# Optimization experiments

Hardware: AMD Instinct MI355X
Metric: run time of the kernel (lower is better)

Reference implementation:

```python
import jax, jax.numpy as jnp
import numpy as np

B, E, K, S, D, H, C = 8192, 8, 2, 32, 3072, 256, 100  # batch, experts, fix_points, img size, flat dim, hidden, classes


def setup_inputs() -> dict:
    key = jax.random.key(0)
    ks = jax.random.split(key, 6)
    return {
        "x": jax.random.normal(ks[0], (B, 3, S, S), jnp.float32),
        "coeffs_t": jax.random.uniform(ks[1], (K,), jnp.float32),
        "router_w": jax.random.normal(ks[2], (K, D, E), jnp.float32) * 0.02,
        "router_b": jnp.zeros((K, E), jnp.float32),
        "w1": jax.random.normal(ks[3], (E, K, D, H), jnp.float32) * 0.02,
        "b1": jnp.zeros((E, K, H), jnp.float32),
        "w2": jax.random.normal(ks[4], (E, K, H, C), jnp.float32) * 0.02,
        "b2": jnp.zeros((E, K, C), jnp.float32),
    }


def reference(x, coeffs_t, router_w, router_b, w1, b1, w2, b2):
    xf = x.reshape(x.shape[0], -1)  # [B, D]
    # Curve parameter blend: W = sum_k coeffs_t[k] * W_k (CurveParameter semantics)
    Wr = jnp.einsum('k,kde->de', coeffs_t, router_w)
    br = jnp.einsum('k,ke->e', coeffs_t, router_b)
    # Router: top-1 expert index per sample
    idx = jnp.argmax(xf @ Wr + br, axis=-1)  # [B] int
    # Blended expert weights
    W1 = jnp.einsum('k,ekdh->edh', coeffs_t, w1)
    B1 = jnp.einsum('k,ekh->eh', coeffs_t, b1)
    W2 = jnp.einsum('k,ekhc->ehc', coeffs_t, w2)
    B2 = jnp.einsum('k,ekc->ec', coeffs_t, b2)
    # Expert MLP (computed for all experts with static shapes, then top-1 gather;
    # identical math to torch's boolean-mask dispatch/scatter)
    h = jax.nn.gelu(jnp.einsum('bd,edh->beh', xf, W1) + B1, approximate=False)  # [B,E,H]
    o = jnp.einsum('beh,ehc->bec', h, W2) + B2  # [B,E,C]
    return jnp.take_along_axis(o, idx[:, None, None], axis=1)[:, 0, :]  # [B,C]
```

## Files before the change

kernel.cpp:

```cpp
#include <hip/hip_runtime.h>
#include <math.h>

#define B_  8192
#define E_  8
#define D_  3072
#define H_  256
#define C_  100
#define DH_ (D_*H_)
#define HC_ (H_*C_)
#define KS_ 8
#define KSEG_ (D_/KS_)
#define NTMAX_ 136

typedef __attribute__((ext_vector_type(4))) float  f32x4;
typedef __attribute__((ext_vector_type(8))) __bf16 bf16x8;
typedef __attribute__((ext_vector_type(8))) unsigned short ush8;
typedef __attribute__((ext_vector_type(4))) unsigned short ush4;

__device__ inline unsigned short bf16_rne(float f) {
    unsigned u = __builtin_bit_cast(unsigned, f);
    unsigned r = (u + 0x7FFFu + ((u >> 16) & 1u)) >> 16;
    return (unsigned short)r;
}
__device__ inline float bf16_f(unsigned short h) {
    unsigned u = ((unsigned)h) << 16;
    return __builtin_bit_cast(float, u);
}

#define MISC_B1_ (E_*H_/4)
#define MISC_B2_ (E_*C_/4)
#define MISC_TOT_ (MISC_B1_ + MISC_B2_ + D_)
__global__ __launch_bounds__(256) void blend_misc_k(
        const float* __restrict__ b1, const float* __restrict__ b2,
        const float* __restrict__ rw, float* __restrict__ B1b,
        float* __restrict__ B2b, double* __restrict__ wsd,
        const float* __restrict__ coeffs) {
    int gid = blockIdx.x * 256 + threadIdx.x;
    float c0 = coeffs[0], c1 = coeffs[1];
    if (gid < MISC_B1_) {
        const float4* p = (const float4*)b1;
        int e = gid / (H_ / 4), r = gid - e * (H_ / 4);
        float4 a = p[(e * 2 + 0) * (H_ / 4) + r];
        float4 bq = p[(e * 2 + 1) * (H_ / 4) + r];
        float4 o;
        o.x = c0 * a.x + c1 * bq.x;
        o.y = c0 * a.y + c1 * bq.y;
        o.z = c0 * a.z + c1 * bq.z;
        o.w = c0 * a.w + c1 * bq.w;
        ((float4*)B1b)[gid] = o;
    } else if (gid < MISC_B1_ + MISC_B2_) {
        int g2 = gid - MISC_B1_;
        const float4* p = (const float4*)b2;
        int e = g2 / (C_ / 4), r = g2 - e * (C_ / 4);
        float4 a = p[(e * 2 + 0) * (C_ / 4) + r];
        float4 bq = p[(e * 2 + 1) * (C_ / 4) + r];
        float4 o;
        o.x = c0 * a.x + c1 * bq.x;
        o.y = c0 * a.y + c1 * bq.y;
        o.z = c0 * a.z + c1 * bq.z;
        o.w = c0 * a.w + c1 * bq.w;
        ((float4*)B2b)[g2] = o;
    } else {
        int d = gid - (MISC_B1_ + MISC_B2_);
        if (d < D_) {
            double c0d = (double)c0, c1d = (double)c1;
            #pragma unroll
            for (int ee = 0; ee < 8; ee++)
                wsd[(size_t)d * 8 + ee] = c0d * (double)rw[(size_t)d * 8 + ee]
                                        + c1d * (double)rw[(size_t)(D_ + d) * 8 + ee];
        }
    }
}

#define TP_ 136
__global__ __launch_bounds__(256) void blendw1t_k(
        const float* __restrict__ w1, unsigned short* __restrict__ Whi,
        unsigned short* __restrict__ Wlo, const float* __restrict__ coeffs) {
    __shared__ unsigned short thi[64 * TP_];
    __shared__ unsigned short tlo[64 * TP_];
    float c0 = coeffs[0], c1 = coeffs[1];
    int t = threadIdx.x;
    int e = blockIdx.z, h0 = blockIdx.y * 64, d0 = blockIdx.x * 128;
    int h = t & 63, dl = t >> 6;
    const float* pa = w1 + ((size_t)(e * 2 + 0) * D_ + d0) * H_ + h0 + h;
    const float* pb = w1 + ((size_t)(e * 2 + 1) * D_ + d0) * H_ + h0 + h;
    for (int it = 0; it < 32; it++) {
        int d = it * 4 + dl;
        float v = c0 * pa[(size_t)d * H_] + c1 * pb[(size_t)d * H_];
        unsigned short hi = bf16_rne(v);
        thi[h * TP_ + d] = hi;
        tlo[h * TP_ + d] = bf16_rne(v - bf16_f(hi));
    }
    __syncthreads();
    #pragma unroll
    for (int it = 0; it < 4; it++) {
        int i = t + it * 256;
        int hh = i >> 4, d8 = (i & 15) * 8;
        size_t g = (size_t)(e * H_ + h0 + hh) * D_ + d0 + d8;
        *(ush8*)(Whi + g) = *(const ush8*)&thi[hh * TP_ + d8];
        *(ush8*)(Wlo + g) = *(const ush8*)&tlo[hh * TP_ + d8];
    }
}

__global__ __launch_bounds__(256) void blendw2t_k(
        const float* __restrict__ w2, unsigned short* __restrict__ W2thi,
        unsigned short* __restrict__ W2tlo, const float* __restrict__ coeffs) {
    float c0 = coeffs[0], c1 = coeffs[1];
    int c = blockIdx.x, e = blockIdx.y, k = threadIdx.x;
    float v = c0 * w2[((size_t)(e * 2 + 0) * H_ + k) * C_ + c]
            + c1 * w2[((size_t)(e * 2 + 1) * H_ + k) * C_ + c];
    unsigned short hi = bf16_rne(v);
    W2thi[(size_t)(e * C_ + c) * H_ + k] = hi;
    W2tlo[(size_t)(e * C_ + c) * H_ + k] = bf16_rne(v - bf16_f(hi));
}

template<int RKS>
__global__ __launch_bounds__(64) void router_v2_t(
        const float* __restrict__ x, const double* __restrict__ wsd,
        double* __restrict__ lpart) {
    const int RSEG = D_ / RKS;
    __shared__ float  xs[64][33];
    __shared__ double wls[32][8];
    int lane = threadIdx.x;
    int row0 = blockIdx.x * 64;
    int kbase = blockIdx.y * RSEG;

    double acc[8] = {0, 0, 0, 0, 0, 0, 0, 0};

    for (int kb = 0; kb < RSEG; kb += 32) {
        #pragma unroll
        for (int it = 0; it < 8; it++) {
            int i = lane + it * 64;
            int r = i >> 3, c4 = i & 7;
            *(float4*)&xs[r][c4 * 4] =
                *(const float4*)(x + (size_t)(row0 + r) * D_ + kbase + kb + c4 * 4);
        }
        #pragma unroll
        for (int it = 0; it < 4; it++) {
            int i = lane + it * 64;
            int k = i >> 3, ee = i & 7;
            wls[k][ee] = wsd[(size_t)(kbase + kb + k) * 8 + ee];
        }
        __syncthreads();
        #pragma unroll
        for (int kk = 0; kk < 32; kk++) {
            double xv = (double)xs[lane][kk];
            double2 w01 = *(const double2*)&wls[kk][0];
            double2 w23 = *(const double2*)&wls[kk][2];
            double2 w45 = *(const double2*)&wls[kk][4];
            double2 w67 = *(const double2*)&wls[kk][6];
            acc[0] = fma(xv, w01.x, acc[0]);
            acc[1] = fma(xv, w01.y, acc[1]);
            acc[2] = fma(xv, w23.x, acc[2]);
            acc[3] = fma(xv, w23.y, acc[3]);
            acc[4] = fma(xv, w45.x, acc[4]);
            acc[5] = fma(xv, w45.y, acc[5]);
            acc[6] = fma(xv, w67.x, acc[6]);
            acc[7] = fma(xv, w67.y, acc[7]);
        }
        __syncthreads();
    }
    size_t base = ((size_t)blockIdx.y * B_ + row0 + lane) * 8;
    #pragma unroll
    for (int ee = 0; ee < 8; ee++) lpart[base + ee] = acc[ee];
}

template<int RKS>
__global__ __launch_bounds__(256) void argmax_t(
        const double* __restrict__ lpart, const float* __restrict__ rb,
        const float* __restrict__ coeffs, int* __restrict__ idx,
        int* __restrict__ cnt) {
    __shared__ int scnt[8];
    int t = threadIdx.x;
    if (t < 8) scnt[t] = 0;
    __syncthreads();
    int b = blockIdx.x * 256 + t;
    double c0 = (double)coeffs[0], c1 = (double)coeffs[1];
    double best = -1e300;
    int bi = 0;
    #pragma unroll
    for (int e = 0; e < 8; e++) {
        double l = c0 * (double)rb[e] + c1 * (double)rb[8 + e];
        #pragma unroll
        for (int s2 = 0; s2 < RKS; s2++)
            l += lpart[((size_t)s2 * B_ + b) * 8 + e];
        if (l > best) { best = l; bi = e; }
    }
    idx[b] = bi;
    atomicAdd(&scnt[bi], 1);
    __syncthreads();
    if (t < 8 && scnt[t] > 0) atomicAdd(&cnt[t], scnt[t]);
}

__global__ void offsets_k(const int* __restrict__ cnt, int* __restrict__ off,
                          int* __restrict__ cursor, int* __restrict__ tmap,
                          int* __restrict__ ntl) {
    if (threadIdx.x == 0) {
        int s = 0;
        for (int e = 0; e < E_; e++) { off[e] = s; cursor[e] = s; s += cnt[e]; }
        int nt = 0;
        for (int e = 0; e < E_; e++)
            for (int t0 = 0; t0 < cnt[e]; t0 += 64)
                tmap[nt++] = (e << 16) | t0;
        ntl[0] = nt;
    }
}

__global__ void scatter_k(const int* __restrict__ idx, int* __restrict__ cursor,
                          int* __restrict__ order) {
    int b = blockIdx.x * blockDim.x + threadIdx.x;
    if (b < B_) {
        int e = idx[b];
        int pos = atomicAdd(&cursor[e], 1);
        order[pos] = (e << 16) | b;
    }
}

template<int MODE>
__global__ __launch_bounds__(256, 3) void gemm1_t(
        const float* __restrict__ x, const unsigned short* __restrict__ Whi,
        const unsigned short* __restrict__ Wlo, const int* __restrict__ order,
        const int* __restrict__ cnt, const int* __restrict__ off,
        const int* __restrict__ tmap, const int* __restrict__ ntl,
        float* __restrict__ dst) {
    int tid = blockIdx.y;
    if (tid >= ntl[0]) return;
    int tm = tmap[tid];
    int e = tm >> 16, tile0 = tm & 0xFFFF;
    int ce = cnt[e];
    int s = blockIdx.x;

    __shared__ int rows[64];
    __shared__ unsigned short xs_hi[64 * 40];
    __shared__ unsigned short xs_lo[64 * 40];
    __shared__ unsigned short ws_hi[256 * 40];
    __shared__ unsigned short ws_lo[256 * 40];

    int t = threadIdx.x;
    if (t < 64) {
        int i = tile0 + t;
        rows[t] = (i < ce) ? (order[off[e] + i] & 0xFFFF) : -1;
    }
    __syncthreads();
    int xrow0 = rows[0];

    int lane = t & 63, w = t >> 6;
    int lr = lane & 15, quad = lane >> 4;
    int kbase = s * KSEG_;

    f32x4 acc[4][4];
    #pragma unroll
    for (int mt = 0; mt < 4; mt++)
        #pragma unroll
        for (int nt = 0; nt < 4; nt++)
            acc[mt][nt] = (f32x4){0.f, 0.f, 0.f, 0.f};

    for (int kb = 0; kb < KSEG_; kb += 32) {
        #pragma unroll
        for (int it = 0; it < 2; it++) {
            int i = t + it * 256;
            int rr = i >> 3, sg = i & 7;
            int row = rows[rr];
            if (row < 0) row = xrow0;
            float4 v = *(const float4*)(x + (size_t)row * D_ + kbase + kb + sg * 4);
            unsigned short h4[4], l4[4];
            float vv[4] = {v.x, v.y, v.z, v.w};
            #pragma unroll
            for (int j = 0; j < 4; j++) {
                unsigned short hi = bf16_rne(vv[j]);
                h4[j] = hi;
                l4[j] = bf16_rne(vv[j] - bf16_f(hi));
            }
            *(ush4*)&xs_hi[rr * 40 + sg * 4] = *(const ush4*)h4;
            *(ush4*)&xs_lo[rr * 40 + sg * 4] = *(const ush4*)l4;
        }
        #pragma unroll
        for (int it = 0; it < 4; it++) {
            int i = t + it * 256;
            int col = i >> 2, ch = i & 3;
            size_t g = (size_t)(e * H_ + col) * D_ + kbase + kb + ch * 8;
            *(ush8*)&ws_hi[col * 40 + ch * 8] = *(const ush8*)(Whi + g);
            *(ush8*)&ws_lo[col * 40 + ch * 8] = *(const ush8*)(Wlo + g);
        }
        __syncthreads();

        bf16x8 ah[4], al[4], bh[4], bl[4];
        #pragma unroll
        for (int mt = 0; mt < 4; mt++) {
            ah[mt] = __builtin_bit_cast(bf16x8, *(const ush8*)&xs_hi[(mt * 16 + lr) * 40 + quad * 8]);
            al[mt] = __builtin_bit_cast(bf16x8, *(const ush8*)&xs_lo[(mt * 16 + lr) * 40 + quad * 8]);
        }
        #pragma unroll
        for (int nt = 0; nt < 4; nt++) {
            int col = w * 64 + nt * 16 + lr;
            bh[nt] = __builtin_bit_cast(bf16x8, *(const ush8*)&ws_hi[col * 40 + quad * 8]);
            bl[nt] = __builtin_bit_cast(bf16x8, *(const ush8*)&ws_lo[col * 40 + quad * 8]);
        }
        #pragma unroll
        for (int mt = 0; mt < 4; mt++)
            #pragma unroll
            for (int nt = 0; nt < 4; nt++) {
                acc[mt][nt] = __builtin_amdgcn_mfma_f32_16x16x32_bf16(ah[mt], bh[nt], acc[mt][nt], 0, 0, 0);
                acc[mt][nt] = __builtin_amdgcn_mfma_f32_16x16x32_bf16(al[mt], bh[nt], acc[mt][nt], 0, 0, 0);
                acc[mt][nt] = __builtin_amdgcn_mfma_f32_16x16x32_bf16(ah[mt], bl[nt], acc[mt][nt], 0, 0, 0);
                acc[mt][nt] = __builtin_amdgcn_mfma_f32_16x16x32_bf16(al[mt], bl[nt], acc[mt][nt], 0, 0, 0);
            }
        __syncthreads();
    }

    size_t p0 = (size_t)off[e] + tile0;
    if (MODE == 1) {
        float* dp = dst + ((size_t)s * B_ + p0) * H_;
        #pragma unroll
        for (int mt = 0; mt < 4; mt++) {
            int rl = mt * 16 + quad * 4;
            #pragma unroll
            for (int nt = 0; nt < 4; nt++) {
                int col = w * 64 + nt * 16 + lr;
                #pragma unroll
                for (int rg = 0; rg < 4; rg++) {
                    if (tile0 + rl + rg < ce)
                        dp[(size_t)(rl + rg) * H_ + col] = acc[mt][nt][rg];
                }
            }
        }
    } else {
        #pragma unroll
        for (int mt = 0; mt < 4; mt++) {
            int rl = mt * 16 + quad * 4;
            #pragma unroll
            for (int nt = 0; nt < 4; nt++) {
                int col = w * 64 + nt * 16 + lr;
                #pragma unroll
                for (int rg = 0; rg < 4; rg++) {
                    if (tile0 + rl + rg < ce)
                        atomicAdd(&dst[(p0 + rl + rg) * H_ + col], acc[mt][nt][rg]);
                }
            }
        }
    }
}

__global__ __launch_bounds__(256) void reduce_gelu_k(
        float* __restrict__ hpart, const float* __restrict__ B1b,
        const int* __restrict__ order) {
    int gid = blockIdx.x * 256 + threadIdx.x;
    int p = gid >> 6, c4 = (gid & 63) * 4;
    int e = order[p] >> 16;
    size_t o = (size_t)p * H_ + c4;
    float4 a = *(const float4*)(hpart + o);
    #pragma unroll
    for (int s2 = 1; s2 < KS_; s2++) {
        float4 b = *(const float4*)(hpart + (size_t)s2 * B_ * H_ + o);
        a.x += b.x; a.y += b.y; a.z += b.z; a.w += b.w;
    }
    const float4 bb = *(const float4*)(B1b + e * H_ + c4);
    float pre[4] = {a.x + bb.x, a.y + bb.y, a.z + bb.z, a.w + bb.w};
    float4 og;
    og.x = 0.5f * pre[0] * (1.0f + erff(pre[0] * 0.70710678118654752440f));
    og.y = 0.5f * pre[1] * (1.0f + erff(pre[1] * 0.70710678118654752440f));
    og.z = 0.5f * pre[2] * (1.0f + erff(pre[2] * 0.70710678118654752440f));
    og.w = 0.5f * pre[3] * (1.0f + erff(pre[3] * 0.70710678118654752440f));
    *(float4*)(hpart + o) = og;
}

__global__ __launch_bounds__(256) void bias_gelu_k(
        float* __restrict__ hws, const float* __restrict__ B1b,
        const int* __restrict__ order) {
    int gid = blockIdx.x * 256 + threadIdx.x;
    int p = gid >> 6, c4 = (gid & 63) * 4;
    int e = order[p] >> 16;
    float4 v = *(const float4*)(hws + (size_t)p * H_ + c4);
    const float4 bb = *(const float4*)(B1b + e * H_ + c4);
    float pre[4] = {v.x + bb.x, v.y + bb.y, v.z + bb.z, v.w + bb.w};
    float4 o;
    o.x = 0.5f * pre[0] * (1.0f + erff(pre[0] * 0.70710678118654752440f));
    o.y = 0.5f * pre[1] * (1.0f + erff(pre[1] * 0.70710678118654752440f));
    o.z = 0.5f * pre[2] * (1.0f + erff(pre[2] * 0.70710678118654752440f));
    o.w = 0.5f * pre[3] * (1.0f + erff(pre[3] * 0.70710678118654752440f));
    *(float4*)(hws + (size_t)p * H_ + c4) = o;
}

__global__ __launch_bounds__(256) void gemm2_k(
        const float* __restrict__ hws,
        const unsigned short* __restrict__ W2thi, const unsigned short* __restrict__ W2tlo,
        const float* __restrict__ B2b, const int* __restrict__ order,
        const int* __restrict__ cnt, const int* __restrict__ off,
        const int* __restrict__ tmap, const int* __restrict__ ntl,
        float* __restrict__ out) {
    int tid = blockIdx.x;
    if (tid >= ntl[0]) return;
    int tm = tmap[tid];
    int e = tm >> 16, tile0 = tm & 0xFFFF;
    int ce = cnt[e];

    __shared__ int rows[64];
    int t = threadIdx.x;
    if (t < 64) {
        int i = tile0 + t;
        rows[t] = (i < ce) ? (order[off[e] + i] & 0xFFFF) : -1;
    }
    __syncthreads();

    int lane = t & 63, w = t >> 6;
    int m = lane & 15, q = lane >> 4;
    int lr = w * 16 + m;
    int p = off[e] + tile0 + ((tile0 + lr < ce) ? lr : 0);

    f32x4 acc[7];
    #pragma unroll
    for (int nt = 0; nt < 7; nt++) acc[nt] = (f32x4){0.f, 0.f, 0.f, 0.f};

    const unsigned short* w2h = W2thi + (size_t)e * C_ * H_;
    const unsigned short* w2l = W2tlo + (size_t)e * C_ * H_;

    #pragma unroll
    for (int s = 0; s < 8; s++) {
        float4 v0 = *(const float4*)(hws + (size_t)p * H_ + s * 32 + q * 8);
        float4 v1 = *(const float4*)(hws + (size_t)p * H_ + s * 32 + q * 8 + 4);
        float f[8] = {v0.x, v0.y, v0.z, v0.w, v1.x, v1.y, v1.z, v1.w};
        unsigned short hh[8], lo[8];
        #pragma unroll
        for (int j = 0; j < 8; j++) {
            unsigned short hi = bf16_rne(f[j]);
            hh[j] = hi;
            lo[j] = bf16_rne(f[j] - bf16_f(hi));
        }
        bf16x8 ah = __builtin_bit_cast(bf16x8, *(const ush8*)hh);
        bf16x8 al = __builtin_bit_cast(bf16x8, *(const ush8*)lo);
        #pragma unroll
        for (int nt = 0; nt < 7; nt++) {
            size_t bo = (size_t)(nt * 16 + m) * H_ + s * 32 + q * 8;
            bf16x8 bh = __builtin_bit_cast(bf16x8, *(const ush8*)(w2h + bo));
            bf16x8 bl = __builtin_bit_cast(bf16x8, *(const ush8*)(w2l + bo));
            acc[nt] = __builtin_amdgcn_mfma_f32_16x16x32_bf16(ah, bh, acc[nt], 0, 0, 0);
            acc[nt] = __builtin_amdgcn_mfma_f32_16x16x32_bf16(al, bh, acc[nt], 0, 0, 0);
            acc[nt] = __builtin_amdgcn_mfma_f32_16x16x32_bf16(ah, bl, acc[nt], 0, 0, 0);
            acc[nt] = __builtin_amdgcn_mfma_f32_16x16x32_bf16(al, bl, acc[nt], 0, 0, 0);
        }
    }

    #pragma unroll
    for (int nt = 0; nt < 7; nt++) {
        int c = nt * 16 + m;
        if (c >= C_) continue;
        float bias = B2b[e * C_ + c];
        #pragma unroll
        for (int i = 0; i < 4; i++) {
            int lrow = w * 16 + q * 4 + i;
            if (tile0 + lrow < ce)
                out[(size_t)rows[lrow] * C_ + c] = acc[nt][i] + bias;
        }
    }
}

extern "C" void kernel_launch(void* const* d_in, const int* in_sizes, int n_in,
                              void* d_out, int out_size, void* d_ws, size_t ws_size,
                              hipStream_t stream) {
    const float* x        = (const float*)d_in[0];
    const float* coeffs   = (const float*)d_in[1];
    const float* router_w = (const float*)d_in[2];
    const float* router_b = (const float*)d_in[3];
    const float* w1       = (const float*)d_in[4];
    const float* b1       = (const float*)d_in[5];
    const float* w2       = (const float*)d_in[6];
    const float* b2       = (const float*)d_in[7];
    float* out = (float*)d_out;

    unsigned short* Whi   = (unsigned short*)d_ws;
    unsigned short* Wlo   = Whi + (size_t)E_ * DH_;
    unsigned short* W2thi = Wlo + (size_t)E_ * DH_;
    unsigned short* W2tlo = W2thi + (size_t)E_ * C_ * H_;
    float* B1b  = (float*)(W2tlo + (size_t)E_ * C_ * H_);
    float* B2b  = B1b + (size_t)E_ * H_;
    int* order  = (int*)(B2b + E_ * C_);
    int* cnt    = order + B_;
    int* off    = cnt + E_;
    int* cursor = off + E_;
    int* tmap   = cursor + E_;
    int* ntl    = tmap + NTMAX_;
    float* hws  = (float*)(ntl + 4);

    size_t prefix_bytes = (size_t)((char*)hws - (char*)d_ws);
    int use_part = (ws_size >= prefix_bytes + (size_t)KS_ * B_ * H_ * sizeof(float) + 256) ? 1 : 0;

    hipMemsetAsync(cnt, 0, 3 * E_ * sizeof(int), stream);

    blendw1t_k<<<dim3(D_ / 128, H_ / 64, E_), 256, 0, stream>>>(w1, Whi, Wlo, coeffs);
    blendw2t_k<<<dim3(C_, E_), 256, 0, stream>>>(w2, W2thi, W2tlo, coeffs);

    if (use_part) {
        double* lpart = (double*)hws;
        double* wsd   = (double*)(hws + (size_t)B_ * H_);
        int*    idx   = (int*)((char*)(hws + (size_t)B_ * H_) + (1u << 20));

        blend_misc_k<<<dim3((MISC_TOT_ + 255) / 256), 256, 0, stream>>>(
            b1, b2, router_w, B1b, B2b, wsd, coeffs);
        router_v2_t<16><<<dim3(B_ / 64, 16), 64, 0, stream>>>(x, wsd, lpart);
        argmax_t<16><<<dim3(B_ / 256), 256, 0, stream>>>(lpart, router_b, coeffs, idx, cnt);
        offsets_k<<<1, 64, 0, stream>>>(cnt, off, cursor, tmap, ntl);
        scatter_k<<<dim3(B_ / 256), 256, 0, stream>>>(idx, cursor, order);

        gemm1_t<1><<<dim3(KS_, NTMAX_), 256, 0, stream>>>(x, Whi, Wlo, order, cnt,
                                                          off, tmap, ntl, hws);
        reduce_gelu_k<<<dim3(B_ * H_ / 4 / 256), 256, 0, stream>>>(hws, B1b, order);
    } else {
        double* lpart = (double*)hws;
        double* wsd   = (double*)((char*)hws + (size_t)8 * B_ * 8 * 8);
        int*    idx   = (int*)((char*)hws + (5u << 20));

        blend_misc_k<<<dim3((MISC_TOT_ + 255) / 256), 256, 0, stream>>>(
            b1, b2, router_w, B1b, B2b, wsd, coeffs);
        router_v2_t<8><<<dim3(B_ / 64, 8), 64, 0, stream>>>(x, wsd, lpart);
        argmax_t<8><<<dim3(B_ / 256), 256, 0, stream>>>(lpart, router_b, coeffs, idx, cnt);
        offsets_k<<<1, 64, 0, stream>>>(cnt, off, cursor, tmap, ntl);
        scatter_k<<<dim3(B_ / 256), 256, 0, stream>>>(idx, cursor, order);

        hipMemsetAsync(hws, 0, (size_t)B_ * H_ * sizeof(float), stream);
        gemm1_t<0><<<dim3(KS_, NTMAX_), 256, 0, stream>>>(x, Whi, Wlo, order, cnt,
                                                          off, tmap, ntl, hws);
        bias_gelu_k<<<dim3(B_ * H_ / 4 / 256), 256, 0, stream>>>(hws, B1b, order);
    }
    gemm2_k<<<dim3(NTMAX_), 256, 0, stream>>>(hws, W2thi, W2tlo, B2b, order,
                                              cnt, off, tmap, ntl, out);
}
```

Measured before the change: 363.1 us.

## Fuse split-K reduce and GELU into gemm2 with 16-row tiles and K-split waves

```diff
diff --git a/kernel.cpp b/kernel.cpp
--- a/kernel.cpp
+++ b/kernel.cpp
@@ -11,6 +11,7 @@
 #define KS_ 8
 #define KSEG_ (D_/KS_)
 #define NTMAX_ 136
+#define NT2MAX_ 528
 
 typedef __attribute__((ext_vector_type(4))) float  f32x4;
 typedef __attribute__((ext_vector_type(8))) __bf16 bf16x8;
@@ -194,7 +195,7 @@
 
 __global__ void offsets_k(const int* __restrict__ cnt, int* __restrict__ off,
                           int* __restrict__ cursor, int* __restrict__ tmap,
-                          int* __restrict__ ntl) {
+                          int* __restrict__ tmap2, int* __restrict__ ntl) {
     if (threadIdx.x == 0) {
         int s = 0;
         for (int e = 0; e < E_; e++) { off[e] = s; cursor[e] = s; s += cnt[e]; }
@@ -203,6 +204,11 @@
             for (int t0 = 0; t0 < cnt[e]; t0 += 64)
                 tmap[nt++] = (e << 16) | t0;
         ntl[0] = nt;
+        int nt2 = 0;
+        for (int e = 0; e < E_; e++)
+            for (int t0 = 0; t0 < cnt[e]; t0 += 16)
+                tmap2[nt2++] = (e << 16) | t0;
+        ntl[1] = nt2;
     }
 }
 
@@ -339,29 +345,6 @@
             }
         }
     }
-}
-
-__global__ __launch_bounds__(256) void reduce_gelu_k(
-        float* __restrict__ hpart, const float* __restrict__ B1b,
-        const int* __restrict__ order) {
-    int gid = blockIdx.x * 256 + threadIdx.x;
-    int p = gid >> 6, c4 = (gid & 63) * 4;
-    int e = order[p] >> 16;
-    size_t o = (size_t)p * H_ + c4;
-    float4 a = *(const float4*)(hpart + o);
-    #pragma unroll
-    for (int s2 = 1; s2 < KS_; s2++) {
-        float4 b = *(const float4*)(hpart + (size_t)s2 * B_ * H_ + o);
-        a.x += b.x; a.y += b.y; a.z += b.z; a.w += b.w;
-    }
-    const float4 bb = *(const float4*)(B1b + e * H_ + c4);
-    float pre[4] = {a.x + bb.x, a.y + bb.y, a.z + bb.z, a.w + bb.w};
-    float4 og;
-    og.x = 0.5f * pre[0] * (1.0f + erff(pre[0] * 0.70710678118654752440f));
-    og.y = 0.5f * pre[1] * (1.0f + erff(pre[1] * 0.70710678118654752440f));
-    og.z = 0.5f * pre[2] * (1.0f + erff(pre[2] * 0.70710678118654752440f));
-    og.w = 0.5f * pre[3] * (1.0f + erff(pre[3] * 0.70710678118654752440f));
-    *(float4*)(hpart + o) = og;
 }
 
 __global__ __launch_bounds__(256) void bias_gelu_k(
@@ -381,22 +364,25 @@
     *(float4*)(hws + (size_t)p * H_ + c4) = o;
 }
 
-__global__ __launch_bounds__(256) void gemm2_k(
-        const float* __restrict__ hws,
+template<int FUSE>
+__global__ __launch_bounds__(256) void gemm2_t(
+        const float* __restrict__ hsrc,
         const unsigned short* __restrict__ W2thi, const unsigned short* __restrict__ W2tlo,
-        const float* __restrict__ B2b, const int* __restrict__ order,
-        const int* __restrict__ cnt, const int* __restrict__ off,
-        const int* __restrict__ tmap, const int* __restrict__ ntl,
-        float* __restrict__ out) {
+        const float* __restrict__ B1b, const float* __restrict__ B2b,
+        const int* __restrict__ order, const int* __restrict__ cnt,
+        const int* __restrict__ off, const int* __restrict__ tmap2,
+        const int* __restrict__ ntl, float* __restrict__ out) {
     int tid = blockIdx.x;
-    if (tid >= ntl[0]) return;
-    int tm = tmap[tid];
+    if (tid >= ntl[1]) return;
+    int tm = tmap2[tid];
     int e = tm >> 16, tile0 = tm & 0xFFFF;
     int ce = cnt[e];
 
-    __shared__ int rows[64];
+    __shared__ int rows[16];
+    __shared__ float red[3][64][28];
+
     int t = threadIdx.x;
-    if (t < 64) {
+    if (t < 16) {
         int i = tile0 + t;
         rows[t] = (i < ce) ? (order[off[e] + i] & 0xFFFF) : -1;
     }
@@ -404,8 +390,7 @@
 
     int lane = t & 63, w = t >> 6;
     int m = lane & 15, q = lane >> 4;
-    int lr = w * 16 + m;
-    int p = off[e] + tile0 + ((tile0 + lr < ce) ? lr : 0);
+    int p = off[e] + tile0 + ((tile0 + m < ce) ? m : 0);
 
     f32x4 acc[7];
     #pragma unroll
@@ -415,10 +400,35 @@
     const unsigned short* w2l = W2tlo + (size_t)e * C_ * H_;
 
     #pragma unroll
-    for (int s = 0; s < 8; s++) {
-        float4 v0 = *(const float4*)(hws + (size_t)p * H_ + s * 32 + q * 8);
-        float4 v1 = *(const float4*)(hws + (size_t)p * H_ + s * 32 + q * 8 + 4);
-        float f[8] = {v0.x, v0.y, v0.z, v0.w, v1.x, v1.y, v1.z, v1.w};
+    for (int si = 0; si < 2; si++) {
+        int s = w * 2 + si;
+        int k0 = s * 32 + q * 8;
+        size_t o = (size_t)p * H_ + k0;
+        float f[8];
+        if (FUSE) {
+            float4 a0 = *(const float4*)(hsrc + o);
+            float4 a1 = *(const float4*)(hsrc + o + 4);
+            #pragma unroll
+            for (int s2 = 1; s2 < KS_; s2++) {
+                const float* sp = hsrc + (size_t)s2 * B_ * H_ + o;
+                float4 b0 = *(const float4*)sp;
+                float4 b1v = *(const float4*)(sp + 4);
+                a0.x += b0.x; a0.y += b0.y; a0.z += b0.z; a0.w += b0.w;
+                a1.x += b1v.x; a1.y += b1v.y; a1.z += b1v.z; a1.w += b1v.w;
+            }
+            float4 bb0 = *(const float4*)(B1b + e * H_ + k0);
+            float4 bb1 = *(const float4*)(B1b + e * H_ + k0 + 4);
+            float pre[8] = {a0.x + bb0.x, a0.y + bb0.y, a0.z + bb0.z, a0.w + bb0.w,
+                            a1.x + bb1.x, a1.y + bb1.y, a1.z + bb1.z, a1.w + bb1.w};
+            #pragma unroll
+            for (int j = 0; j < 8; j++)
+                f[j] = 0.5f * pre[j] * (1.0f + erff(pre[j] * 0.70710678118654752440f));
+        } else {
+            float4 v0 = *(const float4*)(hsrc + o);
+            float4 v1 = *(const float4*)(hsrc + o + 4);
+            f[0] = v0.x; f[1] = v0.y; f[2] = v0.z; f[3] = v0.w;
+            f[4] = v1.x; f[5] = v1.y; f[6] = v1.z; f[7] = v1.w;
+        }
         unsigned short hh[8], lo[8];
         #pragma unroll
         for (int j = 0; j < 8; j++) {
@@ -430,7 +440,7 @@
         bf16x8 al = __builtin_bit_cast(bf16x8, *(const ush8*)lo);
         #pragma unroll
         for (int nt = 0; nt < 7; nt++) {
-            size_t bo = (size_t)(nt * 16 + m) * H_ + s * 32 + q * 8;
+            size_t bo = (size_t)(nt * 16 + m) * H_ + k0;
             bf16x8 bh = __builtin_bit_cast(bf16x8, *(const ush8*)(w2h + bo));
             bf16x8 bl = __builtin_bit_cast(bf16x8, *(const ush8*)(w2l + bo));
             acc[nt] = __builtin_amdgcn_mfma_f32_16x16x32_bf16(ah, bh, acc[nt], 0, 0, 0);
@@ -440,16 +450,32 @@
         }
     }
 
-    #pragma unroll
-    for (int nt = 0; nt < 7; nt++) {
-        int c = nt * 16 + m;
-        if (c >= C_) continue;
-        float bias = B2b[e * C_ + c];
-        #pragma unroll
-        for (int i = 0; i < 4; i++) {
-            int lrow = w * 16 + q * 4 + i;
-            if (tile0 + lrow < ce)
-                out[(size_t)rows[lrow] * C_ + c] = acc[nt][i] + bias;
+    if (w > 0) {
+        #pragma unroll
+        for (int nt = 0; nt < 7; nt++)
+            #pragma unroll
+            for (int i = 0; i < 4; i++)
+                red[w - 1][lane][nt * 4 + i] = acc[nt][i];
+    }
+    __syncthreads();
+    if (w == 0) {
+        #pragma unroll
+        for (int nt = 0; nt < 7; nt++)
+            #pragma unroll
+            for (int i = 0; i < 4; i++)
+                acc[nt][i] = ((acc[nt][i] + red[0][lane][nt * 4 + i])
+                              + red[1][lane][nt * 4 + i]) + red[2][lane][nt * 4 + i];
+        #pragma unroll
+        for (int nt = 0; nt < 7; nt++) {
+            int c = nt * 16 + m;
+            if (c >= C_) continue;
+            float bias = B2b[e * C_ + c];
+            #pragma unroll
+            for (int i = 0; i < 4; i++) {
+                int grow = q * 4 + i;
+                if (tile0 + grow < ce)
+                    out[(size_t)rows[grow] * C_ + c] = acc[nt][i] + bias;
+            }
         }
     }
 }
@@ -478,7 +504,8 @@
     int* off    = cnt + E_;
     int* cursor = off + E_;
     int* tmap   = cursor + E_;
-    int* ntl    = tmap + NTMAX_;
+    int* tmap2  = tmap + NTMAX_;
+    int* ntl    = tmap2 + NT2MAX_;
     float* hws  = (float*)(ntl + 4);
 
     size_t prefix_bytes = (size_t)((char*)hws - (char*)d_ws);
@@ -498,12 +525,13 @@
             b1, b2, router_w, B1b, B2b, wsd, coeffs);
         router_v2_t<16><<<dim3(B_ / 64, 16), 64, 0, stream>>>(x, wsd, lpart);
         argmax_t<16><<<dim3(B_ / 256), 256, 0, stream>>>(lpart, router_b, coeffs, idx, cnt);
-        offsets_k<<<1, 64, 0, stream>>>(cnt, off, cursor, tmap, ntl);
+        offsets_k<<<1, 64, 0, stream>>>(cnt, off, cursor, tmap, tmap2, ntl);
         scatter_k<<<dim3(B_ / 256), 256, 0, stream>>>(idx, cursor, order);
 
         gemm1_t<1><<<dim3(KS_, NTMAX_), 256, 0, stream>>>(x, Whi, Wlo, order, cnt,
                                                           off, tmap, ntl, hws);
-        reduce_gelu_k<<<dim3(B_ * H_ / 4 / 256), 256, 0, stream>>>(hws, B1b, order);
+        gemm2_t<1><<<dim3(NT2MAX_), 256, 0, stream>>>(hws, W2thi, W2tlo, B1b, B2b,
+                                                      order, cnt, off, tmap2, ntl, out);
     } else {
         double* lpart = (double*)hws;
         double* wsd   = (double*)((char*)hws + (size_t)8 * B_ * 8 * 8);
@@ -513,14 +541,14 @@
             b1, b2, router_w, B1b, B2b, wsd, coeffs);
         router_v2_t<8><<<dim3(B_ / 64, 8), 64, 0, stream>>>(x, wsd, lpart);
         argmax_t<8><<<dim3(B_ / 256), 256, 0, stream>>>(lpart, router_b, coeffs, idx, cnt);
-        offsets_k<<<1, 64, 0, stream>>>(cnt, off, cursor, tmap, ntl);
+        offsets_k<<<1, 64, 0, stream>>>(cnt, off, cursor, tmap, tmap2, ntl);
         scatter_k<<<dim3(B_ / 256), 256, 0, stream>>>(idx, cursor, order);
 
         hipMemsetAsync(hws, 0, (size_t)B_ * H_ * sizeof(float), stream);
         gemm1_t<0><<<dim3(KS_, NTMAX_), 256, 0, stream>>>(x, Whi, Wlo, order, cnt,
                                                           off, tmap, ntl, hws);
         bias_gelu_k<<<dim3(B_ * H_ / 4 / 256), 256, 0, stream>>>(hws, B1b, order);
-    }
-    gemm2_k<<<dim3(NTMAX_), 256, 0, stream>>>(hws, W2thi, W2tlo, B2b, order,
-                                              cnt, off, tmap, ntl, out);
-}
+        gemm2_t<0><<<dim3(NT2MAX_), 256, 0, stream>>>(hws, W2thi, W2tlo, B1b, B2b,
+                                                      order, cnt, off, tmap2, ntl, out);
+    }
+}
```

Result: no change. 366.4 us (+0.9%).
